# Performance work log

Measured on AMD Instinct MI355X. Metric: run time of the kernel, lower is better.

The kernel has to match this reference:

```python
import jax, jax.numpy as jnp
import numpy as np

EPS_OT = 0.1        # args.model.ot_reg
N_ITERS = 5         # args.model.ot_transport
COS_EPS = 1e-8      # torch F.cosine_similarity eps
L2_EPS = 1e-12      # torch F.normalize eps
LN_EPS = 1e-5       # nn.LayerNorm default eps
IN_DIM, HID = 768, 256


def setup_inputs() -> dict:
    key = jax.random.key(0)
    ks = jax.random.split(key, 8)
    Ba, Bb, Sa, Sb = 48, 48, 96, 96
    s_in = 1.0 / np.sqrt(IN_DIM)
    return {
        "batch_a": jax.random.normal(ks[0], (Ba, Sa, IN_DIM), jnp.float32),
        "batch_b": jax.random.normal(ks[1], (Bb, Sb, IN_DIM), jnp.float32),
        "Wq": jax.random.normal(ks[2], (IN_DIM, HID), jnp.float32) * s_in,
        "bq": jnp.zeros((HID,), jnp.float32),
        "Wk": jax.random.normal(ks[3], (IN_DIM, HID), jnp.float32) * s_in,
        "bk": jnp.zeros((HID,), jnp.float32),
        "Wv": jax.random.normal(ks[4], (IN_DIM, HID), jnp.float32) * s_in,
        "bv": jnp.zeros((HID,), jnp.float32),
        "ln_g": jnp.ones((HID,), jnp.float32),
        "ln_b": jnp.zeros((HID,), jnp.float32),
    }


def _layernorm(x, g, b):
    mu = jnp.mean(x, axis=-1, keepdims=True)
    var = jnp.var(x, axis=-1, keepdims=True)
    return (x - mu) * jax.lax.rsqrt(var + LN_EPS) * g + b


def _sinkhorn(C):
    # multiplicative Sinkhorn on kernel exp(C/eps); row/col renormalization
    T = jnp.exp(C / EPS_OT)  # [Ba,Bb,Sa,Sb]
    def body(_, T):
        T = T / jnp.sum(T, axis=-1, keepdims=True)
        T = T / jnp.sum(T, axis=-2, keepdims=True)
        return T
    return jax.lax.fori_loop(0, N_ITERS, body, T)


def reference(batch_a, batch_b, Wq, bq, Wk, bk, Wv, bv, ln_g, ln_b):
    q = batch_a @ Wq + bq          # [Ba,Sa,H]
    k = batch_b @ Wk + bk          # [Bb,Sb,H]
    v = batch_b @ Wv + bv          # [Bb,Sb,H]

    # cosine similarity across batches: [Ba,Bb,Sa,Sb]
    qn = q / jnp.maximum(jnp.linalg.norm(q, axis=-1, keepdims=True), COS_EPS)
    kn = k / jnp.maximum(jnp.linalg.norm(k, axis=-1, keepdims=True), COS_EPS)
    C = jnp.einsum('aid,bjd->abij', qn, kn)

    T = jax.lax.stop_gradient(_sinkhorn(C))  # C.detach() in source
    # F.normalize(dim=-1): L2 over last dim
    T = T / jnp.maximum(jnp.linalg.norm(T, axis=-1, keepdims=True), L2_EPS)
    # dropout p=0.0 -> identity (eval)

    attended = jnp.einsum('abij,bjd->abid', T, v) + q[:, None]  # [Ba,Bb,Sa,H]
    return _layernorm(attended, ln_g, ln_b)
```

## Files before the change

### kernel.cpp

```cpp
#include <hip/hip_runtime.h>
#include <hip/hip_bf16.h>

typedef __attribute__((ext_vector_type(4))) float f32x4;
typedef __attribute__((ext_vector_type(2))) float f32x2;
typedef __attribute__((ext_vector_type(8))) short bf16x8;
typedef __attribute__((ext_vector_type(4))) short s16x4;

#define BA 48
#define BB 48
#define SS 96
#define DIN 768
#define HH 256

static __device__ __forceinline__ short f2bf(float f) {
    __hip_bfloat16 h = __float2bfloat16(f);
    return *reinterpret_cast<short*>(&h);
}

static __device__ __forceinline__ f32x4 mfma16(bf16x8 a, bf16x8 b, f32x4 c) {
    return __builtin_amdgcn_mfma_f32_16x16x32_bf16(a, b, c, 0, 0, 0);
}

__global__ __launch_bounds__(256) void wt_kernel(
    const float* __restrict__ Wq, const float* __restrict__ Wk,
    const float* __restrict__ Wv, short* __restrict__ wt) {
    __shared__ float tile[64][65];
    int k0 = blockIdx.x * 64, n0 = blockIdx.y * 64, mat = blockIdx.z;
    const float* W = (mat == 0) ? Wq : (mat == 1) ? Wk : Wv;
    int t = threadIdx.x;
#pragma unroll
    for (int j = 0; j < 16; ++j) {
        int kk = j * 4 + (t >> 6);
        int nn = t & 63;
        tile[kk][nn] = W[(size_t)(k0 + kk) * HH + n0 + nn];
    }
    __syncthreads();
#pragma unroll
    for (int j = 0; j < 4; ++j) {
        int nn = j * 16 + (t >> 4);
        int kk = (t & 15) * 4;
        s16x4 pk;
#pragma unroll
        for (int i = 0; i < 4; ++i) pk[i] = f2bf(tile[kk + i][nn]);
        *reinterpret_cast<s16x4*>(&wt[(size_t)(mat * HH + n0 + nn) * DIN + k0 + kk]) = pk;
    }
}

__global__ __launch_bounds__(256) void xbf_kernel(
    const float* __restrict__ Xa, const float* __restrict__ Xb,
    short* __restrict__ xa, short* __restrict__ xb) {
    size_t i = (size_t)blockIdx.x * 256 + threadIdx.x;
    const float* src;
    short* dst;
    size_t off;
    if (i < 442368) { src = Xa; dst = xa; off = i * 8; }
    else            { src = Xb; dst = xb; off = (i - 442368) * 8; }
    f32x4 a = *reinterpret_cast<const f32x4*>(src + off);
    f32x4 b = *reinterpret_cast<const f32x4*>(src + off + 4);
    bf16x8 o;
    o[0] = f2bf(a[0]); o[1] = f2bf(a[1]); o[2] = f2bf(a[2]); o[3] = f2bf(a[3]);
    o[4] = f2bf(b[0]); o[5] = f2bf(b[1]); o[6] = f2bf(b[2]); o[7] = f2bf(b[3]);
    *reinterpret_cast<bf16x8*>(dst + off) = o;
}

__global__ __launch_bounds__(384) void qkv_kernel(
    const short* __restrict__ xa, const short* __restrict__ xb,
    const float* __restrict__ bq, const float* __restrict__ bk, const float* __restrict__ bv,
    const short* __restrict__ wt,
    float* __restrict__ q_ws, float* __restrict__ k_ws, short* __restrict__ vt_ws) {
    __shared__ short vtile[32][104];

    int bb = blockIdx.x;
    int mat = blockIdx.y;
    int c0 = blockIdx.z * 32;
    int tid = threadIdx.x;
    int wave = tid >> 6, lane = tid & 63;
    int c = lane & 15, g = lane >> 4;

    const short* X = ((mat == 0) ? xa : xb) + (size_t)bb * SS * DIN;
    const short* Wt = wt + (size_t)mat * HH * DIN;
    const float* bias = (mat == 0) ? bq : (mat == 1) ? bk : bv;

    const f32x4 z4 = {0.f, 0.f, 0.f, 0.f};
    f32x4 acc[2];
    acc[0] = z4; acc[1] = z4;

    const short* ap = X + (16 * wave + c) * DIN + g * 8;
    const short* bp = Wt + (c0 + c) * DIN + g * 8;
    for (int kk = 0; kk < DIN; kk += 32) {
        bf16x8 af = *reinterpret_cast<const bf16x8*>(ap + kk);
#pragma unroll
        for (int n = 0; n < 2; ++n) {
            bf16x8 bf = *reinterpret_cast<const bf16x8*>(bp + n * 16 * DIN + kk);
            acc[n] = mfma16(af, bf, acc[n]);
        }
    }
#pragma unroll
    for (int n = 0; n < 2; ++n) {
        float bv_ = bias[c0 + n * 16 + c];
#pragma unroll
        for (int r = 0; r < 4; ++r) acc[n][r] += bv_;
    }

    if (mat < 2) {
        float* dst = (mat == 0) ? q_ws : k_ws;
#pragma unroll
        for (int n = 0; n < 2; ++n)
#pragma unroll
            for (int r = 0; r < 4; ++r)
                dst[(bb * SS + 16 * wave + 4 * g + r) * HH + c0 + n * 16 + c] = acc[n][r];
    } else {
#pragma unroll
        for (int n = 0; n < 2; ++n)
#pragma unroll
            for (int r = 0; r < 4; ++r)
                vtile[n * 16 + c][16 * wave + 4 * g + r] = f2bf(acc[n][r]);
        __syncthreads();
        {
            int t = tid;
            int d = t / 12, ch = t % 12;
            bf16x8 pk = *reinterpret_cast<const bf16x8*>(&vtile[d][ch * 8]);
            *reinterpret_cast<bf16x8*>(vt_ws + ((size_t)(bb * HH) + c0 + d) * SS + ch * 8) = pk;
        }
    }
}

__global__ __launch_bounds__(256) void norm_kernel(
    const float* __restrict__ q_ws, const float* __restrict__ k_ws,
    short* __restrict__ qn_ws, short* __restrict__ kn_ws) {
    int row = blockIdx.x * 4 + (threadIdx.x >> 6);
    int lane = threadIdx.x & 63;
    int isq = (row < 4608);
    const float* src = isq ? q_ws : k_ws;
    short* dst = isq ? qn_ws : kn_ws;
    int r = isq ? row : row - 4608;

    f32x4 v = *reinterpret_cast<const f32x4*>(src + (size_t)r * HH + lane * 4);
    float s = v[0] * v[0] + v[1] * v[1] + v[2] * v[2] + v[3] * v[3];
#pragma unroll
    for (int m = 1; m < 64; m <<= 1) s += __shfl_xor(s, m);
    float inv = 1.0f / fmaxf(sqrtf(s), 1e-8f);
    s16x4 o;
#pragma unroll
    for (int j = 0; j < 4; ++j) o[j] = f2bf(v[j] * inv);
    *reinterpret_cast<s16x4*>(dst + (size_t)r * HH + lane * 4) = o;
}

__global__ __launch_bounds__(256, 2) void sink_kernel(
    const short* __restrict__ qn_ws, const short* __restrict__ kn_ws,
    short* __restrict__ t_ws, int a_off) {
    int wave = threadIdx.x >> 6, lane = threadIdx.x & 63;
    int c = lane & 15, g = lane >> 4;
    int b = blockIdx.x * 4 + wave;
    int al = blockIdx.y;
    int a = al + a_off;

    const short* qbase = qn_ws + (size_t)(a * SS) * HH + c * HH + g * 8;
    const short* kbase = kn_ws + (size_t)(b * SS) * HH + c * HH + g * 8;

    const f32x4 z4 = {0.f, 0.f, 0.f, 0.f};
    f32x4 K[6][6];
#pragma unroll
    for (int ti = 0; ti < 6; ++ti)
#pragma unroll
        for (int tj = 0; tj < 6; ++tj) K[ti][tj] = z4;

#pragma unroll
    for (int kk = 0; kk < 8; ++kk) {
        bf16x8 qf[6];
#pragma unroll
        for (int ti = 0; ti < 6; ++ti)
            qf[ti] = *reinterpret_cast<const bf16x8*>(qbase + ti * 16 * HH + kk * 32);
#pragma unroll
        for (int tj = 0; tj < 6; ++tj) {
            bf16x8 kf = *reinterpret_cast<const bf16x8*>(kbase + tj * 16 * HH + kk * 32);
#pragma unroll
            for (int ti = 0; ti < 6; ++ti)
                K[ti][tj] = mfma16(kf, qf[ti], K[ti][tj]);
        }
    }

#pragma unroll
    for (int ti = 0; ti < 6; ++ti)
#pragma unroll
        for (int tj = 0; tj < 6; ++tj)
#pragma unroll
            for (int r = 0; r < 4; ++r)
                K[ti][tj][r] = exp2f(K[ti][tj][r] * 14.4269504088896341f);

    f32x4 v[6];
#pragma unroll
    for (int tj = 0; tj < 6; ++tj) v[tj] = (f32x4){1.f, 1.f, 1.f, 1.f};
    float u[6];

#pragma unroll 1
    for (int it = 0; it < 5; ++it) {
#pragma unroll
        for (int ti = 0; ti < 6; ++ti) {
            f32x4 p0 = K[ti][0] * v[0] + K[ti][1] * v[1];
            f32x4 p1 = K[ti][2] * v[2] + K[ti][3] * v[3];
            f32x4 p2 = K[ti][4] * v[4] + K[ti][5] * v[5];
            f32x4 p = (p0 + p1) + p2;
            float rs = (p[0] + p[1]) + (p[2] + p[3]);
            rs += __shfl_xor(rs, 16);
            rs += __shfl_xor(rs, 32);
            u[ti] = 1.0f / rs;
        }
#pragma unroll
        for (int tj = 0; tj < 6; ++tj) {
            f32x4 c0 = K[0][tj] * u[0] + K[1][tj] * u[1];
            f32x4 c1 = K[2][tj] * u[2] + K[3][tj] * u[3];
            f32x4 c2 = K[4][tj] * u[4] + K[5][tj] * u[5];
            f32x4 cs = (c0 + c1) + c2;
#pragma unroll
            for (int m = 1; m < 16; m <<= 1)
#pragma unroll
                for (int r = 0; r < 4; ++r) cs[r] += __shfl_xor(cs[r], m);
#pragma unroll
            for (int r = 0; r < 4; ++r) v[tj][r] = 1.0f / cs[r];
        }
    }

    short* tp = t_ws + (size_t)(al * BB + b) * SS * SS;
#pragma unroll
    for (int ti = 0; ti < 6; ++ti) {
        f32x4 w[6];
#pragma unroll
        for (int tj = 0; tj < 6; ++tj) w[tj] = K[ti][tj] * v[tj];
        f32x4 q0 = w[0] * w[0] + w[1] * w[1];
        f32x4 q1 = w[2] * w[2] + w[3] * w[3];
        f32x4 q2 = w[4] * w[4] + w[5] * w[5];
        f32x4 qq = (q0 + q1) + q2;
        float ss = (qq[0] + qq[1]) + (qq[2] + qq[3]);
        ss += __shfl_xor(ss, 16);
        ss += __shfl_xor(ss, 32);
        float linv = 1.0f / fmaxf(sqrtf(ss), 1e-12f);
#pragma unroll
        for (int tj = 0; tj < 6; ++tj) {
            s16x4 pk;
#pragma unroll
            for (int r = 0; r < 4; ++r) pk[r] = f2bf(w[tj][r] * linv);
            *reinterpret_cast<s16x4*>(tp + (16 * ti + c) * SS + 16 * tj + 4 * g) = pk;
        }
    }
}

__global__ __launch_bounds__(768, 6) void pv_kernel(
    const short* __restrict__ t_ws, const short* __restrict__ vt_ws,
    const float* __restrict__ q_ws,
    const float* __restrict__ ln_g, const float* __restrict__ ln_b,
    float* __restrict__ out, int a_off) {
    __shared__ float stats[2][2][SS];
    __shared__ float etile[12][4][136];

    int b = blockIdx.x, al = blockIdx.y;
    int a = al + a_off;
    int tid = threadIdx.x;
    int wave = tid >> 6, lane = tid & 63;
    int rt = wave % 6, h = wave / 6;
    int c = lane & 15, g = lane >> 4;

    const f32x4 z4 = {0.f, 0.f, 0.f, 0.f};
    f32x4 acc[8];
#pragma unroll
    for (int n = 0; n < 8; ++n) acc[n] = z4;

    const short* tp = t_ws + ((size_t)(al * BB + b)) * SS * SS + (16 * rt + c) * SS + g * 8;
    const short* vp = vt_ws + ((size_t)(b * HH) + 128 * h + c) * SS + g * 8;
#pragma unroll
    for (int ks = 0; ks < 3; ++ks) {
        bf16x8 af = *reinterpret_cast<const bf16x8*>(tp + ks * 32);
#pragma unroll
        for (int n = 0; n < 8; ++n) {
            bf16x8 bf = *reinterpret_cast<const bf16x8*>(vp + n * 16 * SS + ks * 32);
            acc[n] = mfma16(af, bf, acc[n]);
        }
    }

    const float* qa = q_ws + (size_t)a * SS * HH + 128 * h;
    int r0 = 16 * rt + 4 * g;
    float s1[4] = {0.f, 0.f, 0.f, 0.f};
    float s2[4] = {0.f, 0.f, 0.f, 0.f};
#pragma unroll
    for (int n = 0; n < 8; ++n)
#pragma unroll
        for (int r = 0; r < 4; ++r) {
            float x = acc[n][r] + qa[(r0 + r) * HH + n * 16 + c];
            acc[n][r] = x;
            s1[r] += x;
            s2[r] += x * x;
        }
#pragma unroll
    for (int m = 1; m < 16; m <<= 1)
#pragma unroll
        for (int r = 0; r < 4; ++r) {
            s1[r] += __shfl_xor(s1[r], m);
            s2[r] += __shfl_xor(s2[r], m);
        }
    if (c == 0) {
#pragma unroll
        for (int r = 0; r < 4; ++r) {
            stats[h][0][r0 + r] = s1[r];
            stats[h][1][r0 + r] = s2[r];
        }
    }
    __syncthreads();
    float mean[4], inv[4];
#pragma unroll
    for (int r = 0; r < 4; ++r) {
        float t1 = stats[0][0][r0 + r] + stats[1][0][r0 + r];
        float t2 = stats[0][1][r0 + r] + stats[1][1][r0 + r];
        mean[r] = t1 * (1.0f / 256.0f);
        float var = t2 * (1.0f / 256.0f) - mean[r] * mean[r];
        inv[r] = rsqrtf(var + 1e-5f);
    }

    f32x2 g2 = *reinterpret_cast<const f32x2*>(ln_g + 128 * h + 2 * lane);
    f32x2 b2 = *reinterpret_cast<const f32x2*>(ln_b + 128 * h + 2 * lane);
    float* ob = out + ((size_t)(a * BB + b)) * SS * HH + 128 * h;
#pragma unroll
    for (int r = 0; r < 4; ++r) {
#pragma unroll
        for (int n = 0; n < 8; ++n)
            etile[wave][g][n * 16 + c] = (acc[n][r] - mean[r]) * inv[r];
#pragma unroll
        for (int t = 0; t < 4; ++t) {
            f32x2 x2 = *reinterpret_cast<const f32x2*>(&etile[wave][t][2 * lane]);
            *reinterpret_cast<f32x2*>(ob + (size_t)(16 * rt + 4 * t + r) * HH + 2 * lane) =
                x2 * g2 + b2;
        }
    }
}

extern "C" void kernel_launch(void* const* d_in, const int* in_sizes, int n_in,
                              void* d_out, int out_size, void* d_ws, size_t ws_size,
                              hipStream_t stream) {
    const float* Xa = (const float*)d_in[0];
    const float* Xb = (const float*)d_in[1];
    const float* Wq = (const float*)d_in[2];
    const float* bq = (const float*)d_in[3];
    const float* Wk = (const float*)d_in[4];
    const float* bk = (const float*)d_in[5];
    const float* Wv = (const float*)d_in[6];
    const float* bv = (const float*)d_in[7];
    const float* ln_g = (const float*)d_in[8];
    const float* ln_b = (const float*)d_in[9];
    float* out = (float*)d_out;

    char* ws = (char*)d_ws;
    short* wt    = (short*)(ws);
    short* xa_bf = (short*)(ws + 1179648);
    short* xb_bf = (short*)(ws + 8257536);
    float* q_ws  = (float*)(ws + 15335424);
    float* k_ws  = (float*)(ws + 20054016);
    short* qn_ws = (short*)(ws + 24772608);
    short* kn_ws = (short*)(ws + 27131904);
    short* vt_ws = (short*)(ws + 29491200);

    const size_t t_full = (size_t)BA * BB * SS * SS * 2;
    size_t t_off = 31850496;
    size_t avail = (ws_size > t_off) ? ws_size - t_off : 0;
    int nch;
    if (avail >= t_full) nch = 1;
    else if (avail >= t_full / 2) nch = 2;
    else if (avail >= t_full / 4) nch = 4;
    else { nch = 4; t_off = 0; }
    short* t_ws = (short*)(ws + t_off);
    int apc = BA / nch;

    wt_kernel<<<dim3(12, 4, 3), dim3(256), 0, stream>>>(Wq, Wk, Wv, wt);
    xbf_kernel<<<dim3(3456), dim3(256), 0, stream>>>(Xa, Xb, xa_bf, xb_bf);
    qkv_kernel<<<dim3(BA, 3, 8), dim3(384), 0, stream>>>(xa_bf, xb_bf, bq, bk, bv, wt,
                                                         q_ws, k_ws, vt_ws);
    norm_kernel<<<dim3(2304), dim3(256), 0, stream>>>(q_ws, k_ws, qn_ws, kn_ws);
    for (int ch = 0; ch < nch; ++ch) {
        sink_kernel<<<dim3(12, apc), dim3(256), 0, stream>>>(qn_ws, kn_ws, t_ws, ch * apc);
        pv_kernel<<<dim3(BB, apc), dim3(768), 0, stream>>>(t_ws, vt_ws, q_ws,
                                                           ln_g, ln_b, out, ch * apc);
    }
}
```

Measured before the change: 241.9 us.

## Split each Sinkhorn 96x96 tile across two waves with LDS row-sum exchange

```diff
diff --git a/kernel.cpp b/kernel.cpp
--- a/kernel.cpp
+++ b/kernel.cpp
@@ -146,24 +146,28 @@
     *reinterpret_cast<s16x4*>(dst + (size_t)r * HH + lane * 4) = o;
 }
 
-__global__ __launch_bounds__(256, 2) void sink_kernel(
+__global__ __launch_bounds__(128) void sink_kernel(
     const short* __restrict__ qn_ws, const short* __restrict__ kn_ws,
     short* __restrict__ t_ws, int a_off) {
+    __shared__ float rex[2][2][6][16];
+    __shared__ float fex[2][6][16];
+
     int wave = threadIdx.x >> 6, lane = threadIdx.x & 63;
     int c = lane & 15, g = lane >> 4;
-    int b = blockIdx.x * 4 + wave;
+    int b = blockIdx.x;
     int al = blockIdx.y;
     int a = al + a_off;
+    int tjo = wave * 3;
 
     const short* qbase = qn_ws + (size_t)(a * SS) * HH + c * HH + g * 8;
-    const short* kbase = kn_ws + (size_t)(b * SS) * HH + c * HH + g * 8;
+    const short* kbase = kn_ws + (size_t)(b * SS) * HH + (tjo * 16 + c) * HH + g * 8;
 
     const f32x4 z4 = {0.f, 0.f, 0.f, 0.f};
-    f32x4 K[6][6];
+    f32x4 K[6][3];
 #pragma unroll
     for (int ti = 0; ti < 6; ++ti)
 #pragma unroll
-        for (int tj = 0; tj < 6; ++tj) K[ti][tj] = z4;
+        for (int tj = 0; tj < 3; ++tj) K[ti][tj] = z4;
 
 #pragma unroll
     for (int kk = 0; kk < 8; ++kk) {
@@ -172,7 +176,7 @@
         for (int ti = 0; ti < 6; ++ti)
             qf[ti] = *reinterpret_cast<const bf16x8*>(qbase + ti * 16 * HH + kk * 32);
 #pragma unroll
-        for (int tj = 0; tj < 6; ++tj) {
+        for (int tj = 0; tj < 3; ++tj) {
             bf16x8 kf = *reinterpret_cast<const bf16x8*>(kbase + tj * 16 * HH + kk * 32);
 #pragma unroll
             for (int ti = 0; ti < 6; ++ti)
@@ -183,31 +187,34 @@
 #pragma unroll
     for (int ti = 0; ti < 6; ++ti)
 #pragma unroll
-        for (int tj = 0; tj < 6; ++tj)
+        for (int tj = 0; tj < 3; ++tj)
 #pragma unroll
             for (int r = 0; r < 4; ++r)
                 K[ti][tj][r] = exp2f(K[ti][tj][r] * 14.4269504088896341f);
 
-    f32x4 v[6];
-#pragma unroll
-    for (int tj = 0; tj < 6; ++tj) v[tj] = (f32x4){1.f, 1.f, 1.f, 1.f};
+    f32x4 v[3];
+#pragma unroll
+    for (int tj = 0; tj < 3; ++tj) v[tj] = (f32x4){1.f, 1.f, 1.f, 1.f};
     float u[6];
 
 #pragma unroll 1
     for (int it = 0; it < 5; ++it) {
+        int buf = it & 1;
 #pragma unroll
         for (int ti = 0; ti < 6; ++ti) {
-            f32x4 p0 = K[ti][0] * v[0] + K[ti][1] * v[1];
-            f32x4 p1 = K[ti][2] * v[2] + K[ti][3] * v[3];
-            f32x4 p2 = K[ti][4] * v[4] + K[ti][5] * v[5];
-            f32x4 p = (p0 + p1) + p2;
+            f32x4 p = K[ti][0] * v[0] + K[ti][1] * v[1];
+            p = p + K[ti][2] * v[2];
             float rs = (p[0] + p[1]) + (p[2] + p[3]);
             rs += __shfl_xor(rs, 16);
             rs += __shfl_xor(rs, 32);
-            u[ti] = 1.0f / rs;
-        }
-#pragma unroll
-        for (int tj = 0; tj < 6; ++tj) {
+            if (g == 0) rex[buf][wave][ti][c] = rs;
+        }
+        __syncthreads();
+#pragma unroll
+        for (int ti = 0; ti < 6; ++ti)
+            u[ti] = 1.0f / (rex[buf][0][ti][c] + rex[buf][1][ti][c]);
+#pragma unroll
+        for (int tj = 0; tj < 3; ++tj) {
             f32x4 c0 = K[0][tj] * u[0] + K[1][tj] * u[1];
             f32x4 c1 = K[2][tj] * u[2] + K[3][tj] * u[3];
             f32x4 c2 = K[4][tj] * u[4] + K[5][tj] * u[5];
@@ -221,26 +228,30 @@
         }
     }
 
-    short* tp = t_ws + (size_t)(al * BB + b) * SS * SS;
 #pragma unroll
     for (int ti = 0; ti < 6; ++ti) {
-        f32x4 w[6];
-#pragma unroll
-        for (int tj = 0; tj < 6; ++tj) w[tj] = K[ti][tj] * v[tj];
-        f32x4 q0 = w[0] * w[0] + w[1] * w[1];
-        f32x4 q1 = w[2] * w[2] + w[3] * w[3];
-        f32x4 q2 = w[4] * w[4] + w[5] * w[5];
-        f32x4 qq = (q0 + q1) + q2;
+        f32x4 w0 = K[ti][0] * v[0];
+        f32x4 w1 = K[ti][1] * v[1];
+        f32x4 w2 = K[ti][2] * v[2];
+        f32x4 qq = w0 * w0 + w1 * w1 + w2 * w2;
         float ss = (qq[0] + qq[1]) + (qq[2] + qq[3]);
         ss += __shfl_xor(ss, 16);
         ss += __shfl_xor(ss, 32);
+        if (g == 0) fex[wave][ti][c] = ss;
+    }
+    __syncthreads();
+    short* tp = t_ws + (size_t)(al * BB + b) * SS * SS;
+#pragma unroll
+    for (int ti = 0; ti < 6; ++ti) {
+        float ss = fex[0][ti][c] + fex[1][ti][c];
         float linv = 1.0f / fmaxf(sqrtf(ss), 1e-12f);
 #pragma unroll
-        for (int tj = 0; tj < 6; ++tj) {
+        for (int tj = 0; tj < 3; ++tj) {
+            f32x4 w = K[ti][tj] * v[tj];
             s16x4 pk;
 #pragma unroll
-            for (int r = 0; r < 4; ++r) pk[r] = f2bf(w[tj][r] * linv);
-            *reinterpret_cast<s16x4*>(tp + (16 * ti + c) * SS + 16 * tj + 4 * g) = pk;
+            for (int r = 0; r < 4; ++r) pk[r] = f2bf(w[r] * linv);
+            *reinterpret_cast<s16x4*>(tp + (16 * ti + c) * SS + 16 * (tjo + tj) + 4 * g) = pk;
         }
     }
 }
@@ -374,7 +385,7 @@
                                                          q_ws, k_ws, vt_ws);
     norm_kernel<<<dim3(2304), dim3(256), 0, stream>>>(q_ws, k_ws, qn_ws, kn_ws);
     for (int ch = 0; ch < nch; ++ch) {
-        sink_kernel<<<dim3(12, apc), dim3(256), 0, stream>>>(qn_ws, kn_ws, t_ws, ch * apc);
+        sink_kernel<<<dim3(BB, apc), dim3(128), 0, stream>>>(qn_ws, kn_ws, t_ws, ch * apc);
         pv_kernel<<<dim3(BB, apc), dim3(768), 0, stream>>>(t_ws, vt_ws, q_ws,
                                                            ln_g, ln_b, out, ch * apc);
     }
```

Result: slower. 270.6 us (+11.9%).

## Store Sinkhorn kernel matrix as packed bf16 in registers, one wave per block

Applied to the files above, without the earlier changes.

```diff
diff --git a/kernel.cpp b/kernel.cpp
--- a/kernel.cpp
+++ b/kernel.cpp
@@ -15,6 +15,17 @@
 static __device__ __forceinline__ short f2bf(float f) {
     __hip_bfloat16 h = __float2bfloat16(f);
     return *reinterpret_cast<short*>(&h);
+}
+
+static __device__ __forceinline__ unsigned pk2bf(float lo, float hi) {
+    return ((unsigned)(unsigned short)f2bf(hi) << 16) | (unsigned)(unsigned short)f2bf(lo);
+}
+
+static __device__ __forceinline__ float ubflo(unsigned p) {
+    return __uint_as_float(p << 16);
+}
+static __device__ __forceinline__ float ubfhi(unsigned p) {
+    return __uint_as_float(p & 0xffff0000u);
 }
 
 static __device__ __forceinline__ f32x4 mfma16(bf16x8 a, bf16x8 b, f32x4 c) {
@@ -146,12 +157,12 @@
     *reinterpret_cast<s16x4*>(dst + (size_t)r * HH + lane * 4) = o;
 }
 
-__global__ __launch_bounds__(256, 2) void sink_kernel(
+__global__ __launch_bounds__(64, 4) void sink_kernel(
     const short* __restrict__ qn_ws, const short* __restrict__ kn_ws,
     short* __restrict__ t_ws, int a_off) {
-    int wave = threadIdx.x >> 6, lane = threadIdx.x & 63;
+    int lane = threadIdx.x;
     int c = lane & 15, g = lane >> 4;
-    int b = blockIdx.x * 4 + wave;
+    int b = blockIdx.x;
     int al = blockIdx.y;
     int a = al + a_off;
 
@@ -159,34 +170,34 @@
     const short* kbase = kn_ws + (size_t)(b * SS) * HH + c * HH + g * 8;
 
     const f32x4 z4 = {0.f, 0.f, 0.f, 0.f};
-    f32x4 K[6][6];
-#pragma unroll
-    for (int ti = 0; ti < 6; ++ti)
-#pragma unroll
-        for (int tj = 0; tj < 6; ++tj) K[ti][tj] = z4;
-
-#pragma unroll
-    for (int kk = 0; kk < 8; ++kk) {
-        bf16x8 qf[6];
-#pragma unroll
-        for (int ti = 0; ti < 6; ++ti)
-            qf[ti] = *reinterpret_cast<const bf16x8*>(qbase + ti * 16 * HH + kk * 32);
+    const float L2E10 = 14.4269504088896341f;
+
+    unsigned Kp[6][6][2];
+
+#pragma unroll
+    for (int ti = 0; ti < 6; ++ti) {
+        f32x4 acc[6];
+#pragma unroll
+        for (int tj = 0; tj < 6; ++tj) acc[tj] = z4;
+#pragma unroll
+        for (int kk = 0; kk < 8; ++kk) {
+            bf16x8 qf = *reinterpret_cast<const bf16x8*>(qbase + ti * 16 * HH + kk * 32);
+#pragma unroll
+            for (int tj = 0; tj < 6; ++tj) {
+                bf16x8 kf = *reinterpret_cast<const bf16x8*>(kbase + tj * 16 * HH + kk * 32);
+                acc[tj] = mfma16(kf, qf, acc[tj]);
+            }
+        }
 #pragma unroll
         for (int tj = 0; tj < 6; ++tj) {
-            bf16x8 kf = *reinterpret_cast<const bf16x8*>(kbase + tj * 16 * HH + kk * 32);
-#pragma unroll
-            for (int ti = 0; ti < 6; ++ti)
-                K[ti][tj] = mfma16(kf, qf[ti], K[ti][tj]);
-        }
-    }
-
-#pragma unroll
-    for (int ti = 0; ti < 6; ++ti)
-#pragma unroll
-        for (int tj = 0; tj < 6; ++tj)
-#pragma unroll
-            for (int r = 0; r < 4; ++r)
-                K[ti][tj][r] = exp2f(K[ti][tj][r] * 14.4269504088896341f);
+            float e0 = exp2f(acc[tj][0] * L2E10);
+            float e1 = exp2f(acc[tj][1] * L2E10);
+            float e2 = exp2f(acc[tj][2] * L2E10);
+            float e3 = exp2f(acc[tj][3] * L2E10);
+            Kp[ti][tj][0] = pk2bf(e0, e1);
+            Kp[ti][tj][1] = pk2bf(e2, e3);
+        }
+    }
 
     f32x4 v[6];
 #pragma unroll
@@ -197,21 +208,27 @@
     for (int it = 0; it < 5; ++it) {
 #pragma unroll
         for (int ti = 0; ti < 6; ++ti) {
-            f32x4 p0 = K[ti][0] * v[0] + K[ti][1] * v[1];
-            f32x4 p1 = K[ti][2] * v[2] + K[ti][3] * v[3];
-            f32x4 p2 = K[ti][4] * v[4] + K[ti][5] * v[5];
-            f32x4 p = (p0 + p1) + p2;
-            float rs = (p[0] + p[1]) + (p[2] + p[3]);
+            float rs0 = 0.f, rs1 = 0.f;
+#pragma unroll
+            for (int tj = 0; tj < 6; ++tj) {
+                rs0 += ubflo(Kp[ti][tj][0]) * v[tj][0] + ubflo(Kp[ti][tj][1]) * v[tj][2];
+                rs1 += ubfhi(Kp[ti][tj][0]) * v[tj][1] + ubfhi(Kp[ti][tj][1]) * v[tj][3];
+            }
+            float rs = rs0 + rs1;
             rs += __shfl_xor(rs, 16);
             rs += __shfl_xor(rs, 32);
             u[ti] = 1.0f / rs;
         }
 #pragma unroll
         for (int tj = 0; tj < 6; ++tj) {
-            f32x4 c0 = K[0][tj] * u[0] + K[1][tj] * u[1];
-            f32x4 c1 = K[2][tj] * u[2] + K[3][tj] * u[3];
-            f32x4 c2 = K[4][tj] * u[4] + K[5][tj] * u[5];
-            f32x4 cs = (c0 + c1) + c2;
+            f32x4 cs = z4;
+#pragma unroll
+            for (int ti = 0; ti < 6; ++ti) {
+                cs[0] += ubflo(Kp[ti][tj][0]) * u[ti];
+                cs[1] += ubfhi(Kp[ti][tj][0]) * u[ti];
+                cs[2] += ubflo(Kp[ti][tj][1]) * u[ti];
+                cs[3] += ubfhi(Kp[ti][tj][1]) * u[ti];
+            }
 #pragma unroll
             for (int m = 1; m < 16; m <<= 1)
 #pragma unroll
@@ -224,22 +241,27 @@
     short* tp = t_ws + (size_t)(al * BB + b) * SS * SS;
 #pragma unroll
     for (int ti = 0; ti < 6; ++ti) {
-        f32x4 w[6];
-#pragma unroll
-        for (int tj = 0; tj < 6; ++tj) w[tj] = K[ti][tj] * v[tj];
-        f32x4 q0 = w[0] * w[0] + w[1] * w[1];
-        f32x4 q1 = w[2] * w[2] + w[3] * w[3];
-        f32x4 q2 = w[4] * w[4] + w[5] * w[5];
-        f32x4 qq = (q0 + q1) + q2;
-        float ss = (qq[0] + qq[1]) + (qq[2] + qq[3]);
+        float ss0 = 0.f, ss1 = 0.f;
+#pragma unroll
+        for (int tj = 0; tj < 6; ++tj) {
+            float t0 = ubflo(Kp[ti][tj][0]) * v[tj][0];
+            float t1 = ubfhi(Kp[ti][tj][0]) * v[tj][1];
+            float t2 = ubflo(Kp[ti][tj][1]) * v[tj][2];
+            float t3 = ubfhi(Kp[ti][tj][1]) * v[tj][3];
+            ss0 += t0 * t0 + t2 * t2;
+            ss1 += t1 * t1 + t3 * t3;
+        }
+        float ss = ss0 + ss1;
         ss += __shfl_xor(ss, 16);
         ss += __shfl_xor(ss, 32);
         float linv = 1.0f / fmaxf(sqrtf(ss), 1e-12f);
 #pragma unroll
         for (int tj = 0; tj < 6; ++tj) {
             s16x4 pk;
-#pragma unroll
-            for (int r = 0; r < 4; ++r) pk[r] = f2bf(w[tj][r] * linv);
+            pk[0] = f2bf(ubflo(Kp[ti][tj][0]) * v[tj][0] * linv);
+            pk[1] = f2bf(ubfhi(Kp[ti][tj][0]) * v[tj][1] * linv);
+            pk[2] = f2bf(ubflo(Kp[ti][tj][1]) * v[tj][2] * linv);
+            pk[3] = f2bf(ubfhi(Kp[ti][tj][1]) * v[tj][3] * linv);
             *reinterpret_cast<s16x4*>(tp + (16 * ti + c) * SS + 16 * tj + 4 * g) = pk;
         }
     }
@@ -374,7 +396,7 @@
                                                          q_ws, k_ws, vt_ws);
     norm_kernel<<<dim3(2304), dim3(256), 0, stream>>>(q_ws, k_ws, qn_ws, kn_ws);
     for (int ch = 0; ch < nch; ++ch) {
-        sink_kernel<<<dim3(12, apc), dim3(256), 0, stream>>>(qn_ws, kn_ws, t_ws, ch * apc);
+        sink_kernel<<<dim3(BB, apc), dim3(64), 0, stream>>>(qn_ws, kn_ws, t_ws, ch * apc);
         pv_kernel<<<dim3(BB, apc), dim3(768), 0, stream>>>(t_ws, vt_ws, q_ws,
                                                            ln_g, ln_b, out, ch * apc);
     }
```

New measurement: 433.4 us. 79.2% more time.

## Compute transposed PV tile so LayerNorm output stores directly as float4

Applied to the files above, without the earlier changes.

```diff
diff --git a/kernel.cpp b/kernel.cpp
--- a/kernel.cpp
+++ b/kernel.cpp
@@ -245,89 +245,92 @@
     }
 }
 
-__global__ __launch_bounds__(768, 6) void pv_kernel(
+__global__ __launch_bounds__(512) void pv_kernel(
     const short* __restrict__ t_ws, const short* __restrict__ vt_ws,
     const float* __restrict__ q_ws,
     const float* __restrict__ ln_g, const float* __restrict__ ln_b,
     float* __restrict__ out, int a_off) {
-    __shared__ float stats[2][2][SS];
-    __shared__ float etile[12][4][136];
+    __shared__ float wstats[8][2][SS];
 
     int b = blockIdx.x, al = blockIdx.y;
     int a = al + a_off;
     int tid = threadIdx.x;
-    int wave = tid >> 6, lane = tid & 63;
-    int rt = wave % 6, h = wave / 6;
+    int w = tid >> 6, lane = tid & 63;
     int c = lane & 15, g = lane >> 4;
+    int d0 = w * 32;
 
     const f32x4 z4 = {0.f, 0.f, 0.f, 0.f};
-    f32x4 acc[8];
-#pragma unroll
-    for (int n = 0; n < 8; ++n) acc[n] = z4;
-
-    const short* tp = t_ws + ((size_t)(al * BB + b)) * SS * SS + (16 * rt + c) * SS + g * 8;
-    const short* vp = vt_ws + ((size_t)(b * HH) + 128 * h + c) * SS + g * 8;
+    f32x4 acc[2][6];
+#pragma unroll
+    for (int dt = 0; dt < 2; ++dt)
+#pragma unroll
+        for (int ti = 0; ti < 6; ++ti) acc[dt][ti] = z4;
+
+    const short* vp = vt_ws + ((size_t)(b * HH) + d0 + c) * SS + g * 8;
+    const short* tp = t_ws + ((size_t)(al * BB + b)) * SS * SS + c * SS + g * 8;
 #pragma unroll
     for (int ks = 0; ks < 3; ++ks) {
-        bf16x8 af = *reinterpret_cast<const bf16x8*>(tp + ks * 32);
-#pragma unroll
-        for (int n = 0; n < 8; ++n) {
-            bf16x8 bf = *reinterpret_cast<const bf16x8*>(vp + n * 16 * SS + ks * 32);
-            acc[n] = mfma16(af, bf, acc[n]);
-        }
-    }
-
-    const float* qa = q_ws + (size_t)a * SS * HH + 128 * h;
-    int r0 = 16 * rt + 4 * g;
-    float s1[4] = {0.f, 0.f, 0.f, 0.f};
-    float s2[4] = {0.f, 0.f, 0.f, 0.f};
-#pragma unroll
-    for (int n = 0; n < 8; ++n)
-#pragma unroll
-        for (int r = 0; r < 4; ++r) {
-            float x = acc[n][r] + qa[(r0 + r) * HH + n * 16 + c];
-            acc[n][r] = x;
-            s1[r] += x;
-            s2[r] += x * x;
-        }
-#pragma unroll
-    for (int m = 1; m < 16; m <<= 1)
-#pragma unroll
-        for (int r = 0; r < 4; ++r) {
-            s1[r] += __shfl_xor(s1[r], m);
-            s2[r] += __shfl_xor(s2[r], m);
-        }
-    if (c == 0) {
-#pragma unroll
-        for (int r = 0; r < 4; ++r) {
-            stats[h][0][r0 + r] = s1[r];
-            stats[h][1][r0 + r] = s2[r];
+        bf16x8 af0 = *reinterpret_cast<const bf16x8*>(vp + ks * 32);
+        bf16x8 af1 = *reinterpret_cast<const bf16x8*>(vp + 16 * SS + ks * 32);
+#pragma unroll
+        for (int ti = 0; ti < 6; ++ti) {
+            bf16x8 bf = *reinterpret_cast<const bf16x8*>(tp + ti * 16 * SS + ks * 32);
+            acc[0][ti] = mfma16(af0, bf, acc[0][ti]);
+            acc[1][ti] = mfma16(af1, bf, acc[1][ti]);
+        }
+    }
+
+    const float* qa = q_ws + (size_t)a * SS * HH;
+#pragma unroll
+    for (int ti = 0; ti < 6; ++ti) {
+        int i = 16 * ti + c;
+        f32x4 q0 = *reinterpret_cast<const f32x4*>(qa + (size_t)i * HH + d0 + 4 * g);
+        f32x4 q1 = *reinterpret_cast<const f32x4*>(qa + (size_t)i * HH + d0 + 16 + 4 * g);
+        f32x4 x0 = acc[0][ti] + q0;
+        f32x4 x1 = acc[1][ti] + q1;
+        acc[0][ti] = x0;
+        acc[1][ti] = x1;
+        f32x4 sv = x0 + x1;
+        f32x4 qv = x0 * x0 + x1 * x1;
+        float l1 = (sv[0] + sv[1]) + (sv[2] + sv[3]);
+        float l2 = (qv[0] + qv[1]) + (qv[2] + qv[3]);
+        l1 += __shfl_xor(l1, 16);
+        l1 += __shfl_xor(l1, 32);
+        l2 += __shfl_xor(l2, 16);
+        l2 += __shfl_xor(l2, 32);
+        if (g == 0) {
+            wstats[w][0][i] = l1;
+            wstats[w][1][i] = l2;
         }
     }
     __syncthreads();
-    float mean[4], inv[4];
-#pragma unroll
-    for (int r = 0; r < 4; ++r) {
-        float t1 = stats[0][0][r0 + r] + stats[1][0][r0 + r];
-        float t2 = stats[0][1][r0 + r] + stats[1][1][r0 + r];
-        mean[r] = t1 * (1.0f / 256.0f);
-        float var = t2 * (1.0f / 256.0f) - mean[r] * mean[r];
-        inv[r] = rsqrtf(var + 1e-5f);
-    }
-
-    f32x2 g2 = *reinterpret_cast<const f32x2*>(ln_g + 128 * h + 2 * lane);
-    f32x2 b2 = *reinterpret_cast<const f32x2*>(ln_b + 128 * h + 2 * lane);
-    float* ob = out + ((size_t)(a * BB + b)) * SS * HH + 128 * h;
-#pragma unroll
-    for (int r = 0; r < 4; ++r) {
-#pragma unroll
-        for (int n = 0; n < 8; ++n)
-            etile[wave][g][n * 16 + c] = (acc[n][r] - mean[r]) * inv[r];
-#pragma unroll
-        for (int t = 0; t < 4; ++t) {
-            f32x2 x2 = *reinterpret_cast<const f32x2*>(&etile[wave][t][2 * lane]);
-            *reinterpret_cast<f32x2*>(ob + (size_t)(16 * rt + 4 * t + r) * HH + 2 * lane) =
-                x2 * g2 + b2;
+
+    f32x4 g4[2], b4[2];
+#pragma unroll
+    for (int dt = 0; dt < 2; ++dt) {
+        g4[dt] = *reinterpret_cast<const f32x4*>(ln_g + d0 + dt * 16 + 4 * g);
+        b4[dt] = *reinterpret_cast<const f32x4*>(ln_b + d0 + dt * 16 + 4 * g);
+    }
+
+    float* ob = out + ((size_t)(a * BB + b)) * SS * HH;
+#pragma unroll
+    for (int ti = 0; ti < 6; ++ti) {
+        int i = 16 * ti + c;
+        float t1 = ((wstats[0][0][i] + wstats[1][0][i]) + (wstats[2][0][i] + wstats[3][0][i])) +
+                   ((wstats[4][0][i] + wstats[5][0][i]) + (wstats[6][0][i] + wstats[7][0][i]));
+        float t2 = ((wstats[0][1][i] + wstats[1][1][i]) + (wstats[2][1][i] + wstats[3][1][i])) +
+                   ((wstats[4][1][i] + wstats[5][1][i]) + (wstats[6][1][i] + wstats[7][1][i]));
+        float mean = t1 * (1.0f / 256.0f);
+        float var = t2 * (1.0f / 256.0f) - mean * mean;
+        float inv = rsqrtf(var + 1e-5f);
+#pragma unroll
+        for (int dt = 0; dt < 2; ++dt) {
+            f32x4 x = acc[dt][ti];
+            f32x4 o;
+#pragma unroll
+            for (int r = 0; r < 4; ++r)
+                o[r] = (x[r] - mean) * inv * g4[dt][r] + b4[dt][r];
+            *reinterpret_cast<f32x4*>(ob + (size_t)i * HH + d0 + dt * 16 + 4 * g) = o;
         }
     }
 }
@@ -375,7 +378,7 @@
     norm_kernel<<<dim3(2304), dim3(256), 0, stream>>>(q_ws, k_ws, qn_ws, kn_ws);
     for (int ch = 0; ch < nch; ++ch) {
         sink_kernel<<<dim3(12, apc), dim3(256), 0, stream>>>(qn_ws, kn_ws, t_ws, ch * apc);
-        pv_kernel<<<dim3(BB, apc), dim3(768), 0, stream>>>(t_ws, vt_ws, q_ws,
+        pv_kernel<<<dim3(BB, apc), dim3(512), 0, stream>>>(t_ws, vt_ws, q_ws,
                                                            ln_g, ln_b, out, ch * apc);
     }
 }
```

Result: no change. 241.1 us (-0.3%).
